# Kernel tuning notes

Hardware: AMD Instinct MI355X
Metric: run time of the kernel (lower is better)

Reference implementation:

```python
import jax, jax.numpy as jnp
import numpy as np

B, N, E, H = 8, 512, 256, 8
HD = E // H
FF = 4 * E
TOPK = max(1, int(N * 0.2))
FW_MAX_DIST = 10      # default of get_shortest_path_matrix
EMB_MAX_IDX = 6       # spd encoder: max_dist(5) + 1
LN_EPS = 1e-5


def _layernorm(x, g, b):
    m = jnp.mean(x, axis=-1, keepdims=True)
    v = jnp.var(x, axis=-1, keepdims=True)
    return (x - m) / jnp.sqrt(v + LN_EPS) * g + b


def setup_inputs() -> dict:
    key = jax.random.key(0)
    ks = jax.random.split(key, 12)
    s = 0.02
    return {
        "x": jax.random.normal(ks[0], (B, N, E), jnp.float32),
        "adj": jax.random.uniform(ks[1], (B, N, N), jnp.float32),
        "emb_spd": (jax.random.normal(ks[2], (EMB_MAX_IDX + 1, H), jnp.float32) * s),
        "w_qkv": jax.random.normal(ks[3], (3 * E, E), jnp.float32) * s,
        "b_qkv": jnp.zeros((3 * E,), jnp.float32),
        "w_out": jax.random.normal(ks[4], (E, E), jnp.float32) * s,
        "b_out": jnp.zeros((E,), jnp.float32),
        "w_ff1": jax.random.normal(ks[5], (FF, E), jnp.float32) * s,
        "b_ff1": jnp.zeros((FF,), jnp.float32),
        "w_ff2": jax.random.normal(ks[6], (E, FF), jnp.float32) * s,
        "b_ff2": jnp.zeros((E,), jnp.float32),
        "g1": jnp.ones((E,), jnp.float32),
        "beta1": jnp.zeros((E,), jnp.float32),
        "g2": jnp.ones((E,), jnp.float32),
        "beta2": jnp.zeros((E,), jnp.float32),
        "w_pool": jax.random.normal(ks[7], (1, E), jnp.float32) * s,
        "b_pool": jnp.zeros((1,), jnp.float32),
    }


def _combined_mask(adj, emb_spd):
    # top-k per row -> binary adjacency via scatter
    _, idx = jax.lax.top_k(adj, TOPK)                       # [B,N,k]
    bi = jnp.arange(B)[:, None, None]
    ri = jnp.arange(N)[None, :, None]
    binary = jnp.zeros_like(adj).at[bi, ri, idx].set(1.0)   # [B,N,N]

    # Floyd-Warshall shortest paths
    dist = jnp.where(binary == 1.0, 1.0, jnp.inf)
    ids = jnp.arange(N)
    dist = dist.at[:, ids, ids].set(0.0)

    def body(k, d):
        return jnp.minimum(d, d[:, :, k][:, :, None] + d[:, k, :][:, None, :])

    dist = jax.lax.fori_loop(0, N, body, dist)
    dist_i = jnp.where(dist > FW_MAX_DIST, -1.0, dist).astype(jnp.int32)

    # spatial bias embedding: indices = clamp(dist+1, 0, max_dist+1)
    sp_idx = jnp.clip(dist_i + 1, 0, EMB_MAX_IDX)           # [B,N,N]
    bias = jnp.transpose(emb_spd[sp_idx], (0, 3, 1, 2))     # [B,H,N,N]

    base = jnp.where(binary == 0.0, -jnp.inf, 0.0)[:, None] # [B,1,N,N]
    return base + bias                                      # [B,H,N,N]


def reference(x, adj, emb_spd, w_qkv, b_qkv, w_out, b_out,
              w_ff1, b_ff1, w_ff2, b_ff2, g1, beta1, g2, beta2,
              w_pool, b_pool):
    mask = _combined_mask(adj, emb_spd)                     # [B,H,N,N]

    # multi-head self-attention (PyTorch MHA, post-norm encoder layer, eval)
    qkv = x @ w_qkv.T + b_qkv                               # [B,N,3E]
    q, k, v = jnp.split(qkv, 3, axis=-1)
    q = q.reshape(B, N, H, HD).transpose(0, 2, 1, 3)
    k = k.reshape(B, N, H, HD).transpose(0, 2, 1, 3)
    v = v.reshape(B, N, H, HD).transpose(0, 2, 1, 3)
    scores = jnp.einsum("bhqd,bhkd->bhqk", q, k) / np.sqrt(HD) + mask
    attn = jax.nn.softmax(scores, axis=-1)
    ctx = jnp.einsum("bhqk,bhkd->bhqd", attn, v)
    ctx = ctx.transpose(0, 2, 1, 3).reshape(B, N, E)
    attn_out = ctx @ w_out.T + b_out

    x1 = _layernorm(x + attn_out, g1, beta1)
    ff = jax.nn.relu(x1 @ w_ff1.T + b_ff1) @ w_ff2.T + b_ff2
    x2 = _layernorm(x1 + ff, g2, beta2)

    # attention pooling over nodes
    w = jax.nn.softmax(jnp.tanh(x2 @ w_pool.T + b_pool), axis=1)  # [B,N,1]
    return jnp.sum(x2 * w, axis=1)                          # [B,E]
```

## Files before the change

kernel.cpp:

```cpp
#include <hip/hip_runtime.h>
#include <math.h>


#define B_ 8
#define N_ 512
#define E_ 256
#define H_ 8
#define HD_ 32
#define TOPK_ 102

typedef __attribute__((ext_vector_type(8))) short bf16x8;
typedef __attribute__((ext_vector_type(4))) float f32x4;

__device__ __forceinline__ unsigned short f2b(float f) {
  unsigned u = __builtin_bit_cast(unsigned, f);
  return (unsigned short)((u + 0x7FFFu + ((u >> 16) & 1u)) >> 16);
}

__device__ __forceinline__ void gload16(const void* g, void* l) {
  __builtin_amdgcn_global_load_lds(
      (const __attribute__((address_space(1))) void*)g,
      (__attribute__((address_space(3))) void*)l, 16, 0, 0);
}

__device__ __forceinline__ uint4 lnpack(const float* __restrict__ p,
                                        const float* __restrict__ g,
                                        const float* __restrict__ b,
                                        float mean, float inv) {
  float4 v0 = *(const float4*)p, v1 = *(const float4*)(p + 4);
  float4 g0 = *(const float4*)g, g1 = *(const float4*)(g + 4);
  float4 b0 = *(const float4*)b, b1 = *(const float4*)(b + 4);
  unsigned short h0 = f2b((v0.x - mean) * inv * g0.x + b0.x);
  unsigned short h1 = f2b((v0.y - mean) * inv * g0.y + b0.y);
  unsigned short h2 = f2b((v0.z - mean) * inv * g0.z + b0.z);
  unsigned short h3 = f2b((v0.w - mean) * inv * g0.w + b0.w);
  unsigned short h4 = f2b((v1.x - mean) * inv * g1.x + b1.x);
  unsigned short h5 = f2b((v1.y - mean) * inv * g1.y + b1.y);
  unsigned short h6 = f2b((v1.z - mean) * inv * g1.z + b1.z);
  unsigned short h7 = f2b((v1.w - mean) * inv * g1.w + b1.w);
  uint4 u;
  u.x = (unsigned)h0 | ((unsigned)h1 << 16);
  u.y = (unsigned)h2 | ((unsigned)h3 << 16);
  u.z = (unsigned)h4 | ((unsigned)h5 << 16);
  u.w = (unsigned)h6 | ((unsigned)h7 << 16);
  return u;
}

__device__ __forceinline__ uint4 cvtpack(const float* __restrict__ p) {
  float4 v0 = *(const float4*)p, v1 = *(const float4*)(p + 4);
  uint4 u;
  u.x = (unsigned)f2b(v0.x) | ((unsigned)f2b(v0.y) << 16);
  u.y = (unsigned)f2b(v0.z) | ((unsigned)f2b(v0.w) << 16);
  u.z = (unsigned)f2b(v1.x) | ((unsigned)f2b(v1.y) << 16);
  u.w = (unsigned)f2b(v1.z) | ((unsigned)f2b(v1.w) << 16);
  return u;
}

__global__ __launch_bounds__(256) void cvt_topk(
    const float* __restrict__ adj, unsigned int* __restrict__ bits,
    const float* __restrict__ wqkv, const float* __restrict__ wout,
    const float* __restrict__ wff1, const float* __restrict__ wff2,
    unsigned short* __restrict__ wqkvb, unsigned short* __restrict__ woutb,
    unsigned short* __restrict__ wff1b, unsigned short* __restrict__ wff2b,
    float* __restrict__ rstat) {
  __shared__ unsigned int hist[1024];
  __shared__ float cval[64];
  __shared__ int cidx[64];
  __shared__ int s_cnt, s_bb, s_need;
  __shared__ unsigned int rowbits[16];
  __shared__ int wsum[4];
  const int t = threadIdx.x;

  if (blockIdx.x >= 4864) {
    int i4 = (blockIdx.x - 4864) * 1024 + t * 4;
    *(float4*)(rstat + i4) = (float4){0.f, 0.f, 0.f, 0.f};
    return;
  }
  if (blockIdx.x >= 4096) {
    int i = ((blockIdx.x - 4096) * 256 + t) * 4;
    const float* src;
    unsigned short* dst;
    int off;
    if (i < 196608)      { src = wqkv; dst = wqkvb; off = i; }
    else if (i < 262144) { src = wout; dst = woutb; off = i - 196608; }
    else if (i < 524288) { src = wff1; dst = wff1b; off = i - 262144; }
    else                 { src = wff2; dst = wff2b; off = i - 524288; }
    float4 v = *(const float4*)(src + off);
    ushort4 o;
    o.x = f2b(v.x); o.y = f2b(v.y); o.z = f2b(v.z); o.w = f2b(v.w);
    *(ushort4*)(dst + off) = o;
    return;
  }
  const int row = blockIdx.x;
  const float* a = adj + (size_t)row * N_;
  const int lane = t & 63;
  const int wave = t >> 6;

  hist[t] = 0u; hist[t + 256] = 0u; hist[t + 512] = 0u; hist[t + 768] = 0u;
  if (t == 0) s_cnt = 0;
  float v0 = a[t];
  float v1 = a[t + 256];
  __syncthreads();
  const int b0 = min(1023, max(0, (int)(v0 * 1024.0f)));
  const int b1 = min(1023, max(0, (int)(v1 * 1024.0f)));
  atomicAdd(&hist[b0], 1u);
  atomicAdd(&hist[b1], 1u);
  __syncthreads();
  const int base = 1020 - 4 * t;
  const int h0 = (int)hist[base], h1 = (int)hist[base + 1];
  const int h2 = (int)hist[base + 2], h3 = (int)hist[base + 3];
  const int g = h0 + h1 + h2 + h3;
  int sc = g;
  #pragma unroll
  for (int off = 1; off < 64; off <<= 1) {
    int y = __shfl_up(sc, off);
    sc += (lane >= off) ? y : 0;
  }
  if (lane == 63) wsum[wave] = sc;
  __syncthreads();
  int wo = 0;
  for (int w = 0; w < wave; w++) wo += wsum[w];
  const int incl = sc + wo;
  const int excl = incl - g;
  if (excl < TOPK_ && incl >= TOPK_) {
    int cum = excl;
    int bb = base;
    const int hh[4] = {h3, h2, h1, h0};
    const int bs[4] = {base + 3, base + 2, base + 1, base};
    #pragma unroll
    for (int u = 0; u < 4; u++) {
      if (cum + hh[u] >= TOPK_) { bb = bs[u]; break; }
      cum += hh[u];
    }
    s_bb = bb;
    s_need = TOPK_ - cum;
  }
  __syncthreads();
  const int bb = s_bb;
  const int need = s_need;
  const bool sel0 = (b0 > bb);
  const bool sel1 = (b1 > bb);
  if (b0 == bb) { int p = atomicAdd(&s_cnt, 1); if (p < 64) { cval[p] = v0; cidx[p] = t; } }
  if (b1 == bb) { int p = atomicAdd(&s_cnt, 1); if (p < 64) { cval[p] = v1; cidx[p] = t + 256; } }
  unsigned long long m0 = __ballot(sel0);
  unsigned long long m1 = __ballot(sel1);
  if (lane == 0) {
    rowbits[2 * wave + 0] = (unsigned int)m0;
    rowbits[2 * wave + 1] = (unsigned int)(m0 >> 32);
    rowbits[8 + 2 * wave + 0] = (unsigned int)m1;
    rowbits[8 + 2 * wave + 1] = (unsigned int)(m1 >> 32);
  }
  __syncthreads();
  const int cnt = min(s_cnt, 64);
  for (int c = t; c < cnt; c += 256) {
    const float v = cval[c];
    const int idx = cidx[c];
    int r = 0;
    for (int j = 0; j < cnt; j++) {
      const float vj = cval[j];
      const int ij = cidx[j];
      if (vj > v || (vj == v && ij < idx)) r++;
    }
    if (r < need) atomicOr(&rowbits[idx >> 5], 1u << (idx & 31));
  }
  __syncthreads();
  if (t < 16) bits[(size_t)row * 16 + t] = rowbits[t];
}

template <int FLAGS, int NT = 64>
__global__ __launch_bounds__(256) void gemm_mfma(
    const unsigned short* __restrict__ A, const float* __restrict__ A32,
    const unsigned short* __restrict__ W, const float* __restrict__ bias,
    const float* __restrict__ res, void* __restrict__ Cout,
    unsigned short* __restrict__ kG, unsigned short* __restrict__ vG,
    float* __restrict__ rstat, const float* __restrict__ lng,
    const float* __restrict__ lnb, int M, int N, int K) {
  constexpr bool A32STAGE = (FLAGS & (16 | 128)) != 0;
  constexpr int NBUF = A32STAGE ? 1 : 2;
  constexpr int NPW = NT / 32;
  constexpr int WDMA = NT / 32;
  __shared__ __align__(16) unsigned short Af[NBUF][4096];
  __shared__ __align__(16) unsigned short Wf[NBUF][NT * 64];
  const int tid = threadIdx.x;
  const int m0 = blockIdx.y * 64, n0 = blockIdx.x * NT;
  const int wave = tid >> 6, lane = tid & 63;
  const int wm = wave & 1, wn = wave >> 1;
  const int q = lane >> 4, l15 = lane & 15;
  const int r = tid >> 2, c0 = tid & 3;

  f32x4 acc[2][NPW];
  #pragma unroll
  for (int i = 0; i < 2; i++)
    #pragma unroll
    for (int j = 0; j < NPW; j++) acc[i][j] = (f32x4){0.f, 0.f, 0.f, 0.f};

  float lmean = 0.f, linv = 0.f;
  if constexpr (FLAGS & 16) {
    float s = rstat[(size_t)(m0 + r) * 2];
    float s2 = rstat[(size_t)(m0 + r) * 2 + 1];
    lmean = s * (1.f / 256.f);
    float var = s2 * (1.f / 256.f) - lmean * lmean;
    linv = rsqrtf(var + 1e-5f);
  }

  const int rl = lane & 15;
  const int colk = ((wave & 1) << 5) + ((lane >> 4) << 3);
  const unsigned short* wp0 =
      W + (size_t)(n0 + ((wave >> 1) << 4) + rl) * K + colk;
  const unsigned short* ap0 = nullptr;
  const unsigned short* ap1 = nullptr;
  if constexpr (!A32STAGE) {
    ap0 = A + (size_t)(m0 + ((wave >> 1) << 4) + rl) * K + colk;
    ap1 = ap0 + (size_t)32 * K;
  }

  if constexpr (A32STAGE) {
    const size_t arow = (size_t)(m0 + r) * K;
    for (int k0 = 0; k0 < K; k0 += 64) {
      uint4 a0, a1;
      if constexpr (FLAGS & 16) {
        a0 = lnpack(A32 + arow + k0 + c0 * 8, lng + k0 + c0 * 8,
                    lnb + k0 + c0 * 8, lmean, linv);
        a1 = lnpack(A32 + arow + k0 + (c0 + 4) * 8, lng + k0 + (c0 + 4) * 8,
                    lnb + k0 + (c0 + 4) * 8, lmean, linv);
      } else {
        a0 = cvtpack(A32 + arow + k0 + c0 * 8);
        a1 = cvtpack(A32 + arow + k0 + (c0 + 4) * 8);
      }
      __syncthreads();
      {
        int kc = c0 >> 2, qq = c0 & 3;
        int s0 = ((r >> 4) * 2 + kc) * 64 + (r & 15) + qq * 16;
        int kc1 = (c0 + 4) >> 2, qq1 = (c0 + 4) & 3;
        int s1 = ((r >> 4) * 2 + kc1) * 64 + (r & 15) + qq1 * 16;
        *(uint4*)(&Af[0][s0 * 8]) = a0;
        *(uint4*)(&Af[0][s1 * 8]) = a1;
      }
      #pragma unroll
      for (int j = 0; j < WDMA; j++)
        gload16(wp0 + (size_t)32 * j * K + k0, &Wf[0][(wave * 64 + j * 256) * 8]);
      __syncthreads();
      #pragma unroll
      for (int kc = 0; kc < 2; kc++) {
        bf16x8 af[2], wf[NPW];
        #pragma unroll
        for (int mt = 0; mt < 2; mt++)
          af[mt] = *(const bf16x8*)(&Af[0][(((wm * 2 + mt) * 2 + kc) * 64 + lane) * 8]);
        #pragma unroll
        for (int nt = 0; nt < NPW; nt++)
          wf[nt] = *(const bf16x8*)(&Wf[0][(((wn * NPW + nt) * 2 + kc) * 64 + lane) * 8]);
        #pragma unroll
        for (int mt = 0; mt < 2; mt++)
          #pragma unroll
          for (int nt = 0; nt < NPW; nt++)
            acc[mt][nt] = __builtin_amdgcn_mfma_f32_16x16x32_bf16(af[mt], wf[nt], acc[mt][nt], 0, 0, 0);
      }
    }
  } else {
    static_assert(NT == 64 || A32STAGE, "DMA path requires NT=64");
    const int nit = K >> 6;
    gload16(ap0, &Af[0][(wave * 64) * 8]);
    gload16(ap1, &Af[0][(256 + wave * 64) * 8]);
    gload16(wp0, &Wf[0][(wave * 64) * 8]);
    gload16(wp0 + (size_t)32 * K, &Wf[0][(256 + wave * 64) * 8]);
    for (int it = 0; it < nit; ++it) {
      const int cur = it & 1;
      if (it + 1 < nit) {
        const int k1 = (it + 1) << 6;
        gload16(ap0 + k1, &Af[cur ^ 1][(wave * 64) * 8]);
        gload16(ap1 + k1, &Af[cur ^ 1][(256 + wave * 64) * 8]);
        gload16(wp0 + k1, &Wf[cur ^ 1][(wave * 64) * 8]);
        gload16(wp0 + (size_t)32 * K + k1, &Wf[cur ^ 1][(256 + wave * 64) * 8]);
        asm volatile("s_waitcnt vmcnt(4)" ::: "memory");
      } else {
        asm volatile("s_waitcnt vmcnt(0)" ::: "memory");
      }
      __builtin_amdgcn_s_barrier();
      __builtin_amdgcn_sched_barrier(0);
      #pragma unroll
      for (int kc = 0; kc < 2; kc++) {
        bf16x8 af[2], wf[2];
        #pragma unroll
        for (int mt = 0; mt < 2; mt++)
          af[mt] = *(const bf16x8*)(&Af[cur][(((wm * 2 + mt) * 2 + kc) * 64 + lane) * 8]);
        #pragma unroll
        for (int nt = 0; nt < 2; nt++)
          wf[nt] = *(const bf16x8*)(&Wf[cur][(((wn * 2 + nt) * 2 + kc) * 64 + lane) * 8]);
        #pragma unroll
        for (int mt = 0; mt < 2; mt++)
          #pragma unroll
          for (int nt = 0; nt < 2; nt++)
            acc[mt][nt] = __builtin_amdgcn_mfma_f32_16x16x32_bf16(af[mt], wf[nt], acc[mt][nt], 0, 0, 0);
      }
      __builtin_amdgcn_sched_barrier(0);
      __builtin_amdgcn_s_barrier();
      __builtin_amdgcn_sched_barrier(0);
    }
  }
  float srow[2][4], sqrow[2][4];
  if constexpr (FLAGS & 8) {
    #pragma unroll
    for (int mt = 0; mt < 2; mt++)
      #pragma unroll
      for (int reg = 0; reg < 4; reg++) { srow[mt][reg] = 0.f; sqrow[mt][reg] = 0.f; }
  }
  #pragma unroll
  for (int nt = 0; nt < NPW; nt++) {
    const int col = n0 + (wn * NPW + nt) * 16 + l15;
    const float bv = bias[col];
    #pragma unroll
    for (int mt = 0; mt < 2; mt++) {
      const int rowb = m0 + (wm * 2 + mt) * 16 + q * 4;
      float ov[4];
      #pragma unroll
      for (int reg = 0; reg < 4; reg++) {
        float o = acc[mt][nt][reg] + bv;
        if constexpr (FLAGS & 64) {
          float rv = res[(size_t)(rowb + reg) * N + col];
          if constexpr (FLAGS & 32) {
            const int rr = rowb + reg;
            float s = rstat[(size_t)rr * 2];
            float s2 = rstat[(size_t)rr * 2 + 1];
            float mn = s * (1.f / 256.f);
            float vv = s2 * (1.f / 256.f) - mn * mn;
            float iv = rsqrtf(vv + 1e-5f);
            rv = (rv - mn) * iv * lng[col] + lnb[col];
          }
          o += rv;
        }
        if constexpr (FLAGS & 1) o = fmaxf(o, 0.f);
        if constexpr (FLAGS & 8) { srow[mt][reg] += o; sqrow[mt][reg] += o * o; }
        ov[reg] = o;
      }
      if constexpr (FLAGS & 4) {
        if (col < 256) {
          #pragma unroll
          for (int reg = 0; reg < 4; reg++)
            ((unsigned short*)Cout)[(size_t)(rowb + reg) * 256 + col] = f2b(ov[reg]);
        } else if (col < 512) {
          const int dfull = col - 256;
          const int hh2 = dfull >> 5, d = dfull & 31;
          const int q2 = d >> 3, sub = d & 7;
          const int bidx = rowb >> 9, j = rowb & 511;
          const int jt = j >> 6, jtile = (j >> 4) & 3, jl = j & 15;
          unsigned short* kp = kG +
              ((size_t)(((bidx * 8 + hh2) * 8 + jt) * 4 + jtile) * 64 + q2 * 16 + jl) * 8 + sub;
          kp[0] = f2b(ov[0]); kp[8] = f2b(ov[1]); kp[16] = f2b(ov[2]); kp[24] = f2b(ov[3]);
        } else {
          const int dfull = col - 512;
          const int hh2 = dfull >> 5, d = dfull & 31;
          const int dt = d >> 4, dl = d & 15;
          const int bidx = rowb >> 9, j = rowb & 511;
          const int jt = j >> 6, jj = j & 63;
          const int kc = jj >> 5, q2 = (jj >> 3) & 3, sub0 = jj & 7;
          ushort4 st;
          st.x = f2b(ov[0]); st.y = f2b(ov[1]); st.z = f2b(ov[2]); st.w = f2b(ov[3]);
          *(ushort4*)(vG +
              ((size_t)(((bidx * 8 + hh2) * 8 + jt) * 4 + dt * 2 + kc) * 64 + q2 * 16 + dl) * 8 + sub0) = st;
        }
      } else if constexpr (FLAGS & 2) {
        #pragma unroll
        for (int reg = 0; reg < 4; reg++)
          ((unsigned short*)Cout)[(size_t)(rowb + reg) * N + col] = f2b(ov[reg]);
      } else {
        #pragma unroll
        for (int reg = 0; reg < 4; reg++)
          ((float*)Cout)[(size_t)(rowb + reg) * N + col] = ov[reg];
      }
    }
  }
  if constexpr (FLAGS & 8) {
    #pragma unroll
    for (int mt = 0; mt < 2; mt++)
      #pragma unroll
      for (int reg = 0; reg < 4; reg++) {
        float s = srow[mt][reg], s2 = sqrow[mt][reg];
        #pragma unroll
        for (int off = 1; off < 16; off <<= 1) {
          s += __shfl_xor(s, off);
          s2 += __shfl_xor(s2, off);
        }
        if (l15 == 0) {
          const int row = m0 + (wm * 2 + mt) * 16 + q * 4 + reg;
          atomicAdd(&rstat[(size_t)row * 2], s);
          atomicAdd(&rstat[(size_t)row * 2 + 1], s2);
        }
      }
  }
}

__global__ __launch_bounds__(256) void attn_mfma(
    const unsigned short* __restrict__ qb, const unsigned short* __restrict__ kG,
    const unsigned short* __restrict__ vG, const unsigned int* __restrict__ bits,
    const float* __restrict__ emb, unsigned short* __restrict__ ctxo) {
  const int bx = blockIdx.x;
  const int ib = bx & 7;
  const int h = (bx >> 3) & 7;
  const int b = bx >> 6;
  const int tid = threadIdx.x;
  const int lane = tid & 63;
  const int wave = tid >> 6;
  const int q = lane >> 4, l15 = lane & 15;

  __shared__ __align__(16) unsigned int mrow[64 * 16];
  __shared__ __align__(16) unsigned short pF[4][2 * 64 * 8];

  {
    int rr = tid >> 2, wq = tid & 3;
    uint4 mw = *(const uint4*)(bits + ((size_t)(b * N_ + ib * 64 + rr)) * 16 + wq * 4);
    *(uint4*)(mrow + rr * 16 + wq * 4) = mw;
  }
  __syncthreads();

  const int i0w = ib * 64 + wave * 16;
  const bf16x8 qf = *(const bf16x8*)(qb + ((size_t)(b * N_ + i0w + l15)) * 256 + h * HD_ + q * 8);
  const float delta = emb[1 * H_ + h] - emb[2 * H_ + h];
  const float scale = 0.17677669529663687f;

  float m_run[4], l_run[4];
  #pragma unroll
  for (int e = 0; e < 4; e++) { m_run[e] = -1e30f; l_run[e] = 0.f; }
  f32x4 cacc[2];
  cacc[0] = (f32x4){0.f, 0.f, 0.f, 0.f};
  cacc[1] = (f32x4){0.f, 0.f, 0.f, 0.f};

  unsigned short* pbase = &pF[wave][0];
  const unsigned short* kb = kG + (size_t)(b * 8 + h) * 8 * 4 * 512;
  const unsigned short* vb = vG + (size_t)(b * 8 + h) * 8 * 4 * 512;

  #pragma unroll 1
  for (int jt = 0; jt < 8; jt++) {
    f32x4 s4[4];
    #pragma unroll
    for (int jtile = 0; jtile < 4; jtile++) {
      bf16x8 kf = *(const bf16x8*)(kb + (size_t)(jt * 4 + jtile) * 512 + lane * 8);
      s4[jtile] = __builtin_amdgcn_mfma_f32_16x16x32_bf16(qf, kf, (f32x4){0.f, 0.f, 0.f, 0.f}, 0, 0, 0);
    }
    unsigned long long mw64[4];
    #pragma unroll
    for (int reg = 0; reg < 4; reg++)
      mw64[reg] = *(const unsigned long long*)(mrow + (wave * 16 + q * 4 + reg) * 16 + jt * 2);
    float smat[4][4];
    #pragma unroll
    for (int jtile = 0; jtile < 4; jtile++) {
      #pragma unroll
      for (int reg = 0; reg < 4; reg++) {
        unsigned int w = (jtile & 2) ? (unsigned int)(mw64[reg] >> 32) : (unsigned int)mw64[reg];
        bool allowed = ((w >> ((jtile & 1) * 16 + l15)) & 1u) != 0u;
        int ig = ib * 64 + wave * 16 + q * 4 + reg;
        int jg = jt * 64 + jtile * 16 + l15;
        float s = s4[jtile][reg] * scale + ((jg == ig) ? delta : 0.f);
        smat[jtile][reg] = allowed ? s : -INFINITY;
      }
    }
    float alpha[4], pmat[4][4];
    #pragma unroll
    for (int reg = 0; reg < 4; reg++) {
      float mloc = fmaxf(fmaxf(smat[0][reg], smat[1][reg]), fmaxf(smat[2][reg], smat[3][reg]));
      #pragma unroll
      for (int off = 1; off < 16; off <<= 1) mloc = fmaxf(mloc, __shfl_xor(mloc, off));
      float mnew = fmaxf(m_run[reg], mloc);
      alpha[reg] = __expf(m_run[reg] - mnew);
      m_run[reg] = mnew;
      float ps = 0.f;
      #pragma unroll
      for (int jtile = 0; jtile < 4; jtile++) {
        float p = __expf(smat[jtile][reg] - mnew);
        pmat[jtile][reg] = p;
        ps += p;
      }
      #pragma unroll
      for (int off = 1; off < 16; off <<= 1) ps += __shfl_xor(ps, off);
      l_run[reg] = l_run[reg] * alpha[reg] + ps;
      cacc[0][reg] *= alpha[reg];
      cacc[1][reg] *= alpha[reg];
    }
    #pragma unroll
    for (int jtile = 0; jtile < 4; jtile++) {
      int j_l = jtile * 16 + l15;
      int sl = ((j_l >> 5) * 64 + ((j_l >> 3) & 3) * 16) * 8 + (j_l & 7);
      #pragma unroll
      for (int reg = 0; reg < 4; reg++)
        pbase[sl + (q * 4 + reg) * 8] = f2b(pmat[jtile][reg]);
    }
    #pragma unroll
    for (int kc = 0; kc < 2; kc++) {
      bf16x8 pf = *(const bf16x8*)(pbase + (kc * 64 + lane) * 8);
      #pragma unroll
      for (int dt = 0; dt < 2; dt++) {
        bf16x8 vf = *(const bf16x8*)(vb + (size_t)(jt * 4 + dt * 2 + kc) * 512 + lane * 8);
        cacc[dt] = __builtin_amdgcn_mfma_f32_16x16x32_bf16(pf, vf, cacc[dt], 0, 0, 0);
      }
    }
  }
  #pragma unroll
  for (int reg = 0; reg < 4; reg++) {
    const float linv = 1.f / l_run[reg];
    const size_t row = (size_t)(b * N_ + i0w + q * 4 + reg);
    #pragma unroll
    for (int dt = 0; dt < 2; dt++)
      ctxo[row * E_ + h * HD_ + dt * 16 + l15] = f2b(cacc[dt][reg] * linv);
  }
}

__global__ __launch_bounds__(256) void ln2pool_kernel(
    const float* __restrict__ t, const float* __restrict__ g,
    const float* __restrict__ be, const float* __restrict__ wp,
    const float* __restrict__ bp, float* __restrict__ partial,
    float* __restrict__ pwsum) {
  __shared__ float sh[4][256];
  __shared__ float she[4];
  const int tid = threadIdx.x;
  const int wave = tid >> 6, lane = tid & 63;
  const int c = blockIdx.x;
  const int col = lane * 4;
  const float4 gv = *(const float4*)(g + col);
  const float4 bev = *(const float4*)(be + col);
  const float4 wpv = *(const float4*)(wp + col);
  const float bpv = bp[0];
  float4 pacc = {0.f, 0.f, 0.f, 0.f};
  float esum = 0.f;
  #pragma unroll
  for (int rr = 0; rr < 2; rr++) {
    const int row = c * 8 + wave * 2 + rr;
    float4 v = *(const float4*)(t + (size_t)row * E_ + col);
    float s = v.x + v.y + v.z + v.w;
    float s2 = v.x * v.x + v.y * v.y + v.z * v.z + v.w * v.w;
    #pragma unroll
    for (int off = 1; off < 64; off <<= 1) {
      s += __shfl_xor(s, off);
      s2 += __shfl_xor(s2, off);
    }
    float mean = s * (1.f / 256.f);
    float var = s2 * (1.f / 256.f) - mean * mean;
    float inv = rsqrtf(var + 1e-5f);
    float4 o;
    o.x = (v.x - mean) * inv * gv.x + bev.x;
    o.y = (v.y - mean) * inv * gv.y + bev.y;
    o.z = (v.z - mean) * inv * gv.z + bev.z;
    o.w = (v.w - mean) * inv * gv.w + bev.w;
    float d = o.x * wpv.x + o.y * wpv.y + o.z * wpv.z + o.w * wpv.w;
    #pragma unroll
    for (int off = 1; off < 64; off <<= 1) d += __shfl_xor(d, off);
    float e = __expf(tanhf(d + bpv));
    pacc.x += e * o.x; pacc.y += e * o.y; pacc.z += e * o.z; pacc.w += e * o.w;
    esum += e;
  }
  *(float4*)(&sh[wave][col]) = pacc;
  if (lane == 0) she[wave] = esum;
  __syncthreads();
  partial[(size_t)c * E_ + tid] =
      sh[0][tid] + sh[1][tid] + sh[2][tid] + sh[3][tid];
  if (tid == 0) pwsum[c] = she[0] + she[1] + she[2] + she[3];
}

__global__ __launch_bounds__(256) void pool_final(
    const float* __restrict__ partial, const float* __restrict__ pwsum,
    float* __restrict__ out) {
  const int b = blockIdx.x;
  const int tid = threadIdx.x;
  float acc = 0.f, ws = 0.f;
  #pragma unroll
  for (int c = 0; c < 64; c++) acc += partial[(size_t)(b * 64 + c) * E_ + tid];
  #pragma unroll
  for (int c = 0; c < 64; c++) ws += pwsum[b * 64 + c];
  out[b * E_ + tid] = acc / ws;
}

extern "C" void kernel_launch(void* const* d_in, const int* in_sizes, int n_in,
                              void* d_out, int out_size, void* d_ws, size_t ws_size,
                              hipStream_t stream) {
  (void)in_sizes; (void)n_in; (void)out_size; (void)ws_size;
  const float* x      = (const float*)d_in[0];
  const float* adj    = (const float*)d_in[1];
  const float* emb    = (const float*)d_in[2];
  const float* w_qkv  = (const float*)d_in[3];
  const float* b_qkv  = (const float*)d_in[4];
  const float* w_out  = (const float*)d_in[5];
  const float* b_out  = (const float*)d_in[6];
  const float* w_ff1  = (const float*)d_in[7];
  const float* b_ff1  = (const float*)d_in[8];
  const float* w_ff2  = (const float*)d_in[9];
  const float* b_ff2  = (const float*)d_in[10];
  const float* g1     = (const float*)d_in[11];
  const float* be1    = (const float*)d_in[12];
  const float* g2     = (const float*)d_in[13];
  const float* be2    = (const float*)d_in[14];
  const float* w_pool = (const float*)d_in[15];
  const float* b_pool = (const float*)d_in[16];

  char* ws = (char*)d_ws;
  unsigned int*   bits  = (unsigned int*)ws;
  unsigned short* qb    = (unsigned short*)(ws + 2359296);
  unsigned short* kG    = (unsigned short*)(ws + 4456448);
  unsigned short* vG    = (unsigned short*)(ws + 6553600);
  unsigned short* ctxb  = (unsigned short*)(ws + 8650752);
  float*          tbuf  = (float*)(ws + 10747904);
  float*          tbuf2 = (float*)(ws + 14942208);
  float*          rstat = (float*)(ws + 19136512);
  unsigned short* hffb  = (unsigned short*)(ws + 21233664);
  unsigned short* wqkvb = (unsigned short*)(ws + 29622272);
  unsigned short* woutb = (unsigned short*)(ws + 30015488);
  unsigned short* wff1b = (unsigned short*)(ws + 30146560);
  unsigned short* wff2b = (unsigned short*)(ws + 30670848);
  float*          partial = (float*)(ws + 31195136);
  float*          pwsum   = (float*)(ws + 31719424);
  float*          outp  = (float*)d_out;

  const int M = B_ * N_;

  cvt_topk<<<4096 + 768 + 8, 256, 0, stream>>>(
      adj, bits, w_qkv, w_out, w_ff1, w_ff2, wqkvb, woutb, wff1b, wff2b,
      rstat);
  gemm_mfma<4 | 128><<<dim3(768 / 64, M / 64), 256, 0, stream>>>(
      nullptr, x, wqkvb, b_qkv, nullptr, qb, kG, vG, nullptr, nullptr,
      nullptr, M, 768, E_);
  attn_mfma<<<B_ * H_ * (N_ / 64), 256, 0, stream>>>(qb, kG, vG, bits, emb, ctxb);
  gemm_mfma<8 | 64><<<dim3(E_ / 64, M / 64), 256, 0, stream>>>(
      ctxb, nullptr, woutb, b_out, x, tbuf, nullptr, nullptr, rstat, nullptr,
      nullptr, M, E_, E_);
  gemm_mfma<1 | 2 | 16, 128><<<dim3(1024 / 128, M / 64), 256, 0, stream>>>(
      nullptr, tbuf, wff1b, b_ff1, nullptr, hffb, nullptr, nullptr, rstat,
      g1, be1, M, 1024, E_);
  gemm_mfma<32 | 64><<<dim3(E_ / 64, M / 64), 256, 0, stream>>>(
      hffb, nullptr, wff2b, b_ff2, tbuf, tbuf2, nullptr, nullptr, rstat,
      g1, be1, M, E_, 1024);
  ln2pool_kernel<<<M / 8, 256, 0, stream>>>(tbuf2, g2, be2, w_pool, b_pool,
                                            partial, pwsum);
  pool_final<<<B_, 256, 0, stream>>>(partial, pwsum, outp);
}
```

Measured before the change: 166.8 us.

## Double-buffer the fp32-staged GEMM path and shrink FF1 tile width

The fp32-input GEMM path (QKV and the LayerNorm-fused FF1 GEMM) now keeps two LDS buffers. It converts or LayerNorms the next A tile and issues the next weight DMA while the current tile is being multiplied, with explicit waitcnt and barriers. This hides global-load latency that the old single-buffer loop exposed. FF1 also moves from 128-wide to 64-wide N tiles, doubling the block count at the cost of re-reading and re-normalizing the A rows more often. Doubling the LDS buffers and the extra barrier per iteration may reduce occupancy.

```diff
diff --git a/kernel.cpp b/kernel.cpp
--- a/kernel.cpp
+++ b/kernel.cpp
@@ -176,11 +176,10 @@
     float* __restrict__ rstat, const float* __restrict__ lng,
     const float* __restrict__ lnb, int M, int N, int K) {
   constexpr bool A32STAGE = (FLAGS & (16 | 128)) != 0;
-  constexpr int NBUF = A32STAGE ? 1 : 2;
   constexpr int NPW = NT / 32;
   constexpr int WDMA = NT / 32;
-  __shared__ __align__(16) unsigned short Af[NBUF][4096];
-  __shared__ __align__(16) unsigned short Wf[NBUF][NT * 64];
+  __shared__ __align__(16) unsigned short Af[2][4096];
+  __shared__ __align__(16) unsigned short Wf[2][NT * 64];
   const int tid = threadIdx.x;
   const int m0 = blockIdx.y * 64, n0 = blockIdx.x * NT;
   const int wave = tid >> 6, lane = tid & 63;
@@ -216,8 +215,12 @@
 
   if constexpr (A32STAGE) {
     const size_t arow = (size_t)(m0 + r) * K;
-    for (int k0 = 0; k0 < K; k0 += 64) {
-      uint4 a0, a1;
+    const int kcA = c0 >> 2, qqA = c0 & 3;
+    const int sA = ((r >> 4) * 2 + kcA) * 64 + (r & 15) + qqA * 16;
+    const int kcB = (c0 + 4) >> 2, qqB = (c0 + 4) & 3;
+    const int sB = ((r >> 4) * 2 + kcB) * 64 + (r & 15) + qqB * 16;
+    const int nit = K >> 6;
+    auto packA = [&](int k0, uint4& a0, uint4& a1) {
       if constexpr (FLAGS & 16) {
         a0 = lnpack(A32 + arow + k0 + c0 * 8, lng + k0 + c0 * 8,
                     lnb + k0 + c0 * 8, lmean, linv);
@@ -227,34 +230,57 @@
         a0 = cvtpack(A32 + arow + k0 + c0 * 8);
         a1 = cvtpack(A32 + arow + k0 + (c0 + 4) * 8);
       }
-      __syncthreads();
-      {
-        int kc = c0 >> 2, qq = c0 & 3;
-        int s0 = ((r >> 4) * 2 + kc) * 64 + (r & 15) + qq * 16;
-        int kc1 = (c0 + 4) >> 2, qq1 = (c0 + 4) & 3;
-        int s1 = ((r >> 4) * 2 + kc1) * 64 + (r & 15) + qq1 * 16;
-        *(uint4*)(&Af[0][s0 * 8]) = a0;
-        *(uint4*)(&Af[0][s1 * 8]) = a1;
-      }
+    };
+    {
+      uint4 a0, a1;
+      packA(0, a0, a1);
+      *(uint4*)(&Af[0][sA * 8]) = a0;
+      *(uint4*)(&Af[0][sB * 8]) = a1;
       #pragma unroll
       for (int j = 0; j < WDMA; j++)
-        gload16(wp0 + (size_t)32 * j * K + k0, &Wf[0][(wave * 64 + j * 256) * 8]);
-      __syncthreads();
+        gload16(wp0 + (size_t)32 * j * K, &Wf[0][(wave * 64 + j * 256) * 8]);
+    }
+    for (int it = 0; it < nit; ++it) {
+      const int cur = it & 1;
+      if (it + 1 < nit) {
+        const int k1 = (it + 1) << 6;
+        uint4 a0, a1;
+        packA(k1, a0, a1);
+        *(uint4*)(&Af[cur ^ 1][sA * 8]) = a0;
+        *(uint4*)(&Af[cur ^ 1][sB * 8]) = a1;
+        #pragma unroll
+        for (int j = 0; j < WDMA; j++)
+          gload16(wp0 + (size_t)32 * j * K + k1,
+                  &Wf[cur ^ 1][(wave * 64 + j * 256) * 8]);
+        asm volatile("s_waitcnt lgkmcnt(0)" ::: "memory");
+        if constexpr (WDMA == 2)
+          asm volatile("s_waitcnt vmcnt(2)" ::: "memory");
+        else
+          asm volatile("s_waitcnt vmcnt(4)" ::: "memory");
+      } else {
+        asm volatile("s_waitcnt vmcnt(0) lgkmcnt(0)" ::: "memory");
+      }
+      __builtin_amdgcn_sched_barrier(0);
+      __builtin_amdgcn_s_barrier();
+      __builtin_amdgcn_sched_barrier(0);
       #pragma unroll
       for (int kc = 0; kc < 2; kc++) {
         bf16x8 af[2], wf[NPW];
         #pragma unroll
         for (int mt = 0; mt < 2; mt++)
-          af[mt] = *(const bf16x8*)(&Af[0][(((wm * 2 + mt) * 2 + kc) * 64 + lane) * 8]);
+          af[mt] = *(const bf16x8*)(&Af[cur][(((wm * 2 + mt) * 2 + kc) * 64 + lane) * 8]);
         #pragma unroll
         for (int nt = 0; nt < NPW; nt++)
-          wf[nt] = *(const bf16x8*)(&Wf[0][(((wn * NPW + nt) * 2 + kc) * 64 + lane) * 8]);
+          wf[nt] = *(const bf16x8*)(&Wf[cur][(((wn * NPW + nt) * 2 + kc) * 64 + lane) * 8]);
         #pragma unroll
         for (int mt = 0; mt < 2; mt++)
           #pragma unroll
           for (int nt = 0; nt < NPW; nt++)
             acc[mt][nt] = __builtin_amdgcn_mfma_f32_16x16x32_bf16(af[mt], wf[nt], acc[mt][nt], 0, 0, 0);
       }
+      __builtin_amdgcn_sched_barrier(0);
+      __builtin_amdgcn_s_barrier();
+      __builtin_amdgcn_sched_barrier(0);
     }
   } else {
     static_assert(NT == 64 || A32STAGE, "DMA path requires NT=64");
@@ -619,7 +645,7 @@
   gemm_mfma<8 | 64><<<dim3(E_ / 64, M / 64), 256, 0, stream>>>(
       ctxb, nullptr, woutb, b_out, x, tbuf, nullptr, nullptr, rstat, nullptr,
       nullptr, M, E_, E_);
-  gemm_mfma<1 | 2 | 16, 128><<<dim3(1024 / 128, M / 64), 256, 0, stream>>>(
+  gemm_mfma<1 | 2 | 16><<<dim3(1024 / 64, M / 64), 256, 0, stream>>>(
       nullptr, tbuf, wff1b, b_ff1, nullptr, hffb, nullptr, nullptr, rstat,
       g1, be1, M, 1024, E_);
   gemm_mfma<32 | 64><<<dim3(E_ / 64, M / 64), 256, 0, stream>>>(
```

Result: slower. 170.7 us (+2.3%).
